# Optimization experiments

Measured on AMD Instinct MI355X. Metric: run time of the kernel, lower is better.

The kernel has to match this reference:

```python
import jax, jax.numpy as jnp
import numpy as np

N_NODES = 100000
N_EDGES = 1600000
IN_CH, HID_CH, OUT_CH = 128, 128, 64


def gcn_conv(x, edge_index, W, b, n_nodes):
    """PyG-style GCNConv: add self-loops, symmetric deg^-1/2 normalization,
    linear transform, scatter-add aggregation, bias."""
    src, dst = edge_index[0], edge_index[1]
    loop = jnp.arange(n_nodes, dtype=src.dtype)
    src = jnp.concatenate([src, loop])
    dst = jnp.concatenate([dst, loop])
    # degree computed on destination side (includes self-loops)
    deg = jax.ops.segment_sum(jnp.ones_like(dst, dtype=x.dtype), dst,
                              num_segments=n_nodes)
    dinv = jnp.where(deg > 0, jax.lax.rsqrt(deg), jnp.zeros_like(deg))
    norm = dinv[src] * dinv[dst]            # [E+N]
    h = x @ W                               # [N, out] transform before aggregate
    msg = h[src] * norm[:, None]            # [E+N, out] gathered+scaled messages
    out = jax.ops.segment_sum(msg, dst, num_segments=n_nodes)
    return out + b


def setup_inputs() -> dict:
    key = jax.random.key(0)
    ks = jax.random.split(key, 6)
    x = jax.random.normal(ks[0], (N_NODES, IN_CH), dtype=jnp.float32)
    pos_edge_index = jax.random.randint(ks[1], (2, N_EDGES), 0, N_NODES, dtype=jnp.int64)
    neg_edge_index = jax.random.randint(ks[2], (2, N_EDGES), 0, N_NODES, dtype=jnp.int64)
    # Glorot-ish init for weights
    W1 = jax.random.normal(ks[3], (IN_CH, HID_CH), dtype=jnp.float32) / np.sqrt(IN_CH)
    b1 = jnp.zeros((HID_CH,), dtype=jnp.float32)
    W2 = jax.random.normal(ks[4], (HID_CH, OUT_CH), dtype=jnp.float32) / np.sqrt(HID_CH)
    b2 = jnp.zeros((OUT_CH,), dtype=jnp.float32)
    return {"x": x, "pos_edge_index": pos_edge_index,
            "neg_edge_index": neg_edge_index,
            "W1": W1, "b1": b1, "W2": W2, "b2": b2}


def reference(x, pos_edge_index, neg_edge_index, W1, b1, W2, b2):
    n = x.shape[0]
    # encode: conv1 -> relu -> conv2 (message passing uses pos_edge_index)
    h = gcn_conv(x, pos_edge_index, W1, b1, n)
    h = jax.nn.relu(h)
    z = gcn_conv(h, pos_edge_index, W2, b2, n)
    # decode: gather node pairs, elementwise mul, sum over feature dim
    pos_pred = jnp.sum(z[pos_edge_index[0]] * z[pos_edge_index[1]], axis=1)
    neg_pred = jnp.sum(z[neg_edge_index[0]] * z[neg_edge_index[1]], axis=1)
    return (pos_pred, neg_pred)
```

## Files before the change

kernel.cpp:

```cpp
#include <hip/hip_runtime.h>


#define IC1 128
#define OC1 128
#define OC2 64

#define BSH    9
#define BNODES (1 << BSH)
#define NBMAX  512
#define CHB    4096
#define CHH    4096

typedef unsigned int u32;
typedef unsigned short u16;
typedef __attribute__((ext_vector_type(8))) short short8v;
typedef __attribute__((ext_vector_type(4))) float f32x4;

__device__ __forceinline__ u16 f2bf(float f) {
  u32 u = __float_as_uint(f);
  u32 r = (u + 0x7fffu + ((u >> 16) & 1u)) >> 16;
  return (u16)r;
}
__device__ __forceinline__ u32 pack2bf(float lo, float hi) {
  return (u32)f2bf(lo) | ((u32)f2bf(hi) << 16);
}
__device__ __forceinline__ float bflo(u32 w) { return __uint_as_float(w << 16); }
__device__ __forceinline__ float bfhi(u32 w) { return __uint_as_float(w & 0xffff0000u); }

__device__ __forceinline__ int getIdx(const void* p, long long i, int is64) {
  return is64 ? (int)((const long long*)p)[i] : ((const int*)p)[i];
}

__global__ void k_detect(const void* pei, long long E, int n_nodes, int* flagbuf,
                         int* bcnt, int* gcur0, int NB) {
  __shared__ int bad;
  if (threadIdx.x == 0) bad = 0;
  __syncthreads();
  long long cnt = E < 4096 ? E : 4096;
  const unsigned long long* p64 = (const unsigned long long*)pei;
  for (long long i = threadIdx.x; i < cnt; i += blockDim.x)
    if (p64[i] >= (unsigned long long)n_nodes) bad = 1;
  for (int i = threadIdx.x; i < NB; i += blockDim.x) { bcnt[i] = 0; gcur0[i] = 0; }
  __syncthreads();
  if (threadIdx.x == 0) flagbuf[0] = bad ? 0 : 1;
}

__global__ __launch_bounds__(256) void k_hist(const void* pei, long long E,
                                              const int* flagbuf, int* bcnt, int NB) {
  __shared__ int h[NBMAX];
  int f = flagbuf[0];
  for (int i = threadIdx.x; i < NB; i += 256) h[i] = 0;
  __syncthreads();
  long long e0 = (long long)blockIdx.x * CHH;
  long long e1 = min(E, e0 + CHH);
  for (long long e = e0 + threadIdx.x; e < e1; e += 256)
    atomicAdd(&h[getIdx(pei, E + e, f) >> BSH], 1);
  __syncthreads();
  for (int i = threadIdx.x; i < NB; i += 256)
    if (h[i]) atomicAdd(&bcnt[i], h[i]);
}

__global__ __launch_bounds__(256) void k_bin(const void* pei, long long E,
                                             const int* flagbuf, const int* bcnt,
                                             int* gcur0, u32* binned, int NB) {
  __shared__ u32 stage[CHB];
  __shared__ int h[NBMAX], lofs[NBMAX + 1], cur[NBMAX], gofs[NBMAX], gboff[NBMAX];
  __shared__ int sa[256];
  __shared__ int carryS;
  int f = flagbuf[0];
  int tid = threadIdx.x;
  for (int i = tid; i < NB; i += 256) h[i] = 0;
  if (tid == 0) carryS = 0;
  __syncthreads();
  long long e0 = (long long)blockIdx.x * CHB;
  long long e1 = min(E, e0 + CHB);
  int cc = (int)(e1 - e0);
  for (long long e = e0 + tid; e < e1; e += 256)
    atomicAdd(&h[getIdx(pei, E + e, f) >> BSH], 1);
  __syncthreads();
  for (int base = 0; base < NB; base += 256) {
    int i = base + tid;
    int v = (i < NB) ? h[i] : 0;
    sa[tid] = v;
    __syncthreads();
    for (int off = 1; off < 256; off <<= 1) {
      int t = (tid >= off) ? sa[tid - off] : 0;
      __syncthreads();
      sa[tid] += t;
      __syncthreads();
    }
    int exc = sa[tid] - v + carryS;
    if (i < NB) { lofs[i] = exc; cur[i] = exc; }
    __syncthreads();
    if (tid == 255) carryS += sa[255];
    __syncthreads();
  }
  if (tid == 0) { lofs[NB] = cc; carryS = 0; }
  __syncthreads();
  for (int base = 0; base < NB; base += 256) {
    int i = base + tid;
    int v = (i < NB) ? bcnt[i] : 0;
    sa[tid] = v;
    __syncthreads();
    for (int off = 1; off < 256; off <<= 1) {
      int t = (tid >= off) ? sa[tid - off] : 0;
      __syncthreads();
      sa[tid] += t;
      __syncthreads();
    }
    int exc = sa[tid] - v + carryS;
    if (i < NB) gboff[i] = exc;
    __syncthreads();
    if (tid == 255) carryS += sa[255];
    __syncthreads();
  }
  for (long long e = e0 + tid; e < e1; e += 256) {
    int s = getIdx(pei, e, f);
    int d = getIdx(pei, E + e, f);
    int b = d >> BSH;
    int p = atomicAdd(&cur[b], 1);
    stage[p] = (u32)s | ((u32)(d & (BNODES - 1)) << 20);
  }
  __syncthreads();
  for (int b = tid; b < NB; b += 256) {
    int cnt = cur[b] - lofs[b];
    gofs[b] = cnt ? (gboff[b] + atomicAdd(&gcur0[b], cnt) - lofs[b]) : 0;
  }
  __syncthreads();
  for (int i = tid; i < cc; i += 256) {
    int lo = 0, hi = NB;
    while (hi - lo > 1) {
      int mid = (lo + hi) >> 1;
      if (lofs[mid] <= i) lo = mid; else hi = mid;
    }
    binned[(long long)i + gofs[lo]] = stage[i];
  }
}

__global__ __launch_bounds__(512) void k_fill2(const u32* __restrict__ binned,
                                               const int* __restrict__ bcnt,
                                               float* __restrict__ dinv,
                                               int* __restrict__ rowst,
                                               u32* __restrict__ csr, int N, int NB) {
  __shared__ int cnt[BNODES], sa[BNODES], sb[BNODES], cursor[BNODES];
  __shared__ int redu[8];
  __shared__ int baseS;
  int b = blockIdx.x;
  int v0 = b << BSH;
  int nv = min(BNODES, N - v0);
  int tid = threadIdx.x;
  int part = 0;
  for (int i = tid; i < b; i += 512) part += bcnt[i];
  #pragma unroll
  for (int off = 32; off; off >>= 1) part += __shfl_down(part, off);
  if ((tid & 63) == 0) redu[tid >> 6] = part;
  for (int i = tid; i < BNODES; i += 512) cnt[i] = 0;
  __syncthreads();
  if (tid == 0) {
    int s = 0;
    #pragma unroll
    for (int w = 0; w < 8; ++w) s += redu[w];
    baseS = s;
  }
  __syncthreads();
  int base = baseS;
  int j1 = base + bcnt[b];
  for (int j = base + tid; j < j1; j += 512)
    atomicAdd(&cnt[binned[j] >> 20], 1);
  __syncthreads();
  sa[tid] = cnt[tid];
  __syncthreads();
  int* A = sa; int* B = sb;
  #pragma unroll 1
  for (int off = 1; off < BNODES; off <<= 1) {
    B[tid] = A[tid] + ((tid >= off) ? A[tid - off] : 0);
    __syncthreads();
    int* t = A; A = B; B = t;
  }
  if (tid < nv) {
    int c = cnt[tid];
    int exc = A[tid] - c;
    rowst[v0 + tid] = base + exc;
    cursor[tid] = exc;
    dinv[v0 + tid] = rsqrtf((float)(c + 1));
  }
  if (b == NB - 1 && tid == 0) rowst[N] = j1;
  __syncthreads();
  for (int j = base + tid; j < j1; j += 512) {
    u32 u = binned[j];
    int p = atomicAdd(&cursor[u >> 20], 1);
    csr[base + p] = u & 0xFFFFFu;
  }
}

__global__ void k_prepw(const float* __restrict__ W1, const float* __restrict__ W2,
                        u16* __restrict__ Wt1, u16* __restrict__ Wt2) {
  int i = blockIdx.x * blockDim.x + threadIdx.x;
  if (i < 128 * OC1) {
    int k = i / OC1, c = i % OC1;
    Wt1[c * 128 + k] = f2bf(W1[i]);
  } else {
    int j = i - 128 * OC1;
    if (j < 128 * OC2) {
      int k = j / OC2, c = j % OC2;
      Wt2[c * 128 + k] = f2bf(W2[j]);
    }
  }
}

template<int OC, bool BF16IN>
__global__ __launch_bounds__(256) void k_gemm_mfma(const void* __restrict__ xin,
                                                   const u16* __restrict__ Wt,
                                                   u16* __restrict__ t, int N) {
  constexpr int CT = OC / 16;
  constexpr int LW = 136;
  __shared__ u16 xs[128][LW];
  const int tid = threadIdx.x;
  const int lane = tid & 63, wv = tid >> 6;
  const long long rowBase = (long long)blockIdx.x * 128;

  if constexpr (BF16IN) {
    const u16* xg = (const u16*)xin;
    #pragma unroll
    for (int i = tid; i < 128 * 16; i += 256) {
      int r = i >> 4, c = i & 15;
      uint4 v = make_uint4(0u, 0u, 0u, 0u);
      if (rowBase + r < N) v = ((const uint4*)(xg + (rowBase + r) * IC1))[c];
      *(uint4*)&xs[r][c * 8] = v;
    }
  } else {
    const float* xg = (const float*)xin;
    #pragma unroll
    for (int i = tid; i < 128 * 16; i += 256) {
      int r = i >> 4, c = i & 15;
      uint4 o = make_uint4(0u, 0u, 0u, 0u);
      if (rowBase + r < N) {
        const float4* src = (const float4*)(xg + (rowBase + r) * IC1 + c * 8);
        float4 a = src[0], bq = src[1];
        o.x = pack2bf(a.x, a.y);  o.y = pack2bf(a.z, a.w);
        o.z = pack2bf(bq.x, bq.y); o.w = pack2bf(bq.z, bq.w);
      }
      *(uint4*)&xs[r][c * 8] = o;
    }
  }
  __syncthreads();

  const int frow = lane & 15, fk = (lane >> 4) * 8;
  short8v a[2][4];
  #pragma unroll
  for (int rt = 0; rt < 2; ++rt)
    #pragma unroll
    for (int kq = 0; kq < 4; ++kq)
      a[rt][kq] = *(const short8v*)&xs[wv * 32 + rt * 16 + frow][kq * 32 + fk];

  f32x4 acc[2][CT];
  #pragma unroll
  for (int ct = 0; ct < CT; ++ct) {
    acc[0][ct] = (f32x4){0.f, 0.f, 0.f, 0.f};
    acc[1][ct] = (f32x4){0.f, 0.f, 0.f, 0.f};
    #pragma unroll
    for (int kq = 0; kq < 4; ++kq) {
      short8v bfrag = *(const short8v*)(Wt + (ct * 16 + frow) * 128 + kq * 32 + fk);
      acc[0][ct] = __builtin_amdgcn_mfma_f32_16x16x32_bf16(a[0][kq], bfrag, acc[0][ct], 0, 0, 0);
      acc[1][ct] = __builtin_amdgcn_mfma_f32_16x16x32_bf16(a[1][kq], bfrag, acc[1][ct], 0, 0, 0);
    }
  }

  const int crow0 = (lane >> 4) * 4, ccol = lane & 15;
  #pragma unroll
  for (int rt = 0; rt < 2; ++rt)
    #pragma unroll
    for (int ct = 0; ct < CT; ++ct)
      #pragma unroll
      for (int r = 0; r < 4; ++r) {
        long long row = rowBase + wv * 32 + rt * 16 + crow0 + r;
        if (row < N) t[row * OC + ct * 16 + ccol] = f2bf(acc[rt][ct][r]);
      }
}

template<int CH>
__global__ __launch_bounds__(256) void k_agg(const u16* __restrict__ t,
                                             u16* __restrict__ out,
                                             const float* __restrict__ dinv,
                                             const int* __restrict__ rowst,
                                             const u32* __restrict__ csr,
                                             const float* __restrict__ bias,
                                             int N, int relu) {
  constexpr int G   = CH / 8;
  constexpr int EPI = 64 / G;
  long long wid = ((long long)blockIdx.x * blockDim.x + threadIdx.x) >> 6;
  int lane = threadIdx.x & 63;
  if (wid >= N) return;
  int v = (int)wid;
  int sub = lane / G;
  int cl  = lane % G;
  float dv = dinv[v];
  float selfw = (sub == 0) ? dv * dv : 0.f;
  float acc[8];
  {
    uint4 u = ((const uint4*)(t + (long long)v * CH))[cl];
    acc[0] = bflo(u.x) * selfw; acc[1] = bfhi(u.x) * selfw;
    acc[2] = bflo(u.y) * selfw; acc[3] = bfhi(u.y) * selfw;
    acc[4] = bflo(u.z) * selfw; acc[5] = bfhi(u.z) * selfw;
    acc[6] = bflo(u.w) * selfw; acc[7] = bfhi(u.w) * selfw;
  }
  int st = rowst[v];
  int cnt = rowst[v + 1] - st;
  for (int base = 0; base < cnt; base += 64) {
    int m = min(64, cnt - base);
    int s = 0; float w = 0.f;
    if (lane < m) { s = (int)csr[st + base + lane]; w = dinv[s] * dv; }
    int iters = (m + EPI - 1) / EPI;
    #pragma unroll 4
    for (int j = 0; j < iters; ++j) {
      int src  = __shfl(s, j * EPI + sub);
      float ww = __shfl(w, j * EPI + sub);
      uint4 u = ((const uint4*)(t + (long long)src * CH))[cl];
      acc[0] += bflo(u.x) * ww; acc[1] += bfhi(u.x) * ww;
      acc[2] += bflo(u.y) * ww; acc[3] += bfhi(u.y) * ww;
      acc[4] += bflo(u.z) * ww; acc[5] += bfhi(u.z) * ww;
      acc[6] += bflo(u.w) * ww; acc[7] += bfhi(u.w) * ww;
    }
  }
  #pragma unroll
  for (int off = G; off < 64; off <<= 1) {
    #pragma unroll
    for (int i = 0; i < 8; ++i) acc[i] += __shfl_xor(acc[i], off);
  }
  if (sub == 0) {
    float4 b0 = ((const float4*)bias)[cl * 2];
    float4 b1 = ((const float4*)bias)[cl * 2 + 1];
    float o[8] = {acc[0] + b0.x, acc[1] + b0.y, acc[2] + b0.z, acc[3] + b0.w,
                  acc[4] + b1.x, acc[5] + b1.y, acc[6] + b1.z, acc[7] + b1.w};
    if (relu) {
      #pragma unroll
      for (int i = 0; i < 8; ++i) o[i] = fmaxf(o[i], 0.f);
    }
    uint4 w4;
    w4.x = pack2bf(o[0], o[1]); w4.y = pack2bf(o[2], o[3]);
    w4.z = pack2bf(o[4], o[5]); w4.w = pack2bf(o[6], o[7]);
    ((uint4*)(out + (long long)v * CH))[cl] = w4;
  }
}

__global__ __launch_bounds__(256) void k_decode(const u16* __restrict__ z,
                                                const void* pei, const void* nei,
                                                float* __restrict__ out,
                                                long long E, const int* flagbuf) {
  int f = flagbuf[0];
  long long g = ((long long)blockIdx.x * blockDim.x + threadIdx.x) >> 3;
  int wi = threadIdx.x & 7;
  if (g >= 2 * E) return;
  const void* ei = (g < E) ? pei : nei;
  long long e = (g < E) ? g : g - E;
  int s = getIdx(ei, e, f);
  int d = getIdx(ei, E + e, f);
  uint4 a = ((const uint4*)(z + (long long)s * OC2))[wi];
  uint4 b = ((const uint4*)(z + (long long)d * OC2))[wi];
  float p = bflo(a.x) * bflo(b.x) + bfhi(a.x) * bfhi(b.x)
          + bflo(a.y) * bflo(b.y) + bfhi(a.y) * bfhi(b.y)
          + bflo(a.z) * bflo(b.z) + bfhi(a.z) * bfhi(b.z)
          + bflo(a.w) * bflo(b.w) + bfhi(a.w) * bfhi(b.w);
  p += __shfl_xor(p, 4);
  p += __shfl_xor(p, 2);
  p += __shfl_xor(p, 1);
  if (wi == 0) out[g] = p;
}

extern "C" void kernel_launch(void* const* d_in, const int* in_sizes, int n_in,
                              void* d_out, int out_size, void* d_ws, size_t ws_size,
                              hipStream_t stream) {
  const float* x  = (const float*)d_in[0];
  const void*  pei = d_in[1];
  const void*  nei = d_in[2];
  const float* W1 = (const float*)d_in[3];
  const float* b1 = (const float*)d_in[4];
  const float* W2 = (const float*)d_in[5];
  const float* b2 = (const float*)d_in[6];
  float* out = (float*)d_out;

  const int       N  = in_sizes[0] / IC1;
  const long long E  = in_sizes[1] / 2;
  const int       NB = (N + BNODES - 1) >> BSH;

  char* p = (char*)d_ws;
  auto carve = [&](size_t bytes) { char* r = p; p += ((bytes + 255) & ~(size_t)255); return r; };
  int*   flagbuf = (int*)  carve(8);
  float* dinv    = (float*)carve((size_t)N * 4);
  int*   rowst   = (int*)  carve((size_t)(N + 1) * 4);
  int*   bcnt    = (int*)  carve((size_t)NB * 4);
  int*   gcur0   = (int*)  carve((size_t)NB * 4);
  u32*   binned  = (u32*)  carve((size_t)E * 4);
  u32*   csr     = (u32*)  carve((size_t)E * 4);
  u16*   Wt1     = (u16*)  carve((size_t)128 * OC1 * 2);
  u16*   Wt2     = (u16*)  carve((size_t)128 * OC2 * 2);
  u16*   bufA    = (u16*)  carve((size_t)N * IC1 * 2);
  u16*   bufB    = (u16*)  carve((size_t)N * IC1 * 2);

  const int B = 256;

  k_detect<<<1, B, 0, stream>>>(pei, E, N, flagbuf, bcnt, gcur0, NB);
  k_hist<<<dim3((unsigned)((E + CHH - 1) / CHH)), B, 0, stream>>>(pei, E, flagbuf,
                                                                  bcnt, NB);
  k_bin<<<dim3((unsigned)((E + CHB - 1) / CHB)), B, 0, stream>>>(pei, E, flagbuf,
                                                                 bcnt, gcur0,
                                                                 binned, NB);
  k_fill2<<<dim3(NB), 512, 0, stream>>>(binned, bcnt, dinv, rowst, csr, N, NB);

  k_prepw<<<dim3((128 * (OC1 + OC2) + B - 1) / B), B, 0, stream>>>(W1, W2, Wt1, Wt2);

  k_gemm_mfma<OC1, false><<<dim3((N + 127) / 128), B, 0, stream>>>(x, Wt1, bufA, N);
  k_agg<OC1><<<dim3((N + 3) / 4), B, 0, stream>>>(bufA, bufB, dinv, rowst,
                                                  csr, b1, N, 1);

  k_gemm_mfma<OC2, true><<<dim3((N + 127) / 128), B, 0, stream>>>(bufB, Wt2, bufA, N);
  k_agg<OC2><<<dim3((N + 3) / 4), B, 0, stream>>>(bufA, bufB, dinv, rowst,
                                                  csr, b2, N, 0);

  long long groups = 2 * E;
  dim3 gD((unsigned)((groups * 8 + B - 1) / B));
  k_decode<<<gD, B, 0, stream>>>(bufB, pei, nei, out, E, flagbuf);
}
```

Measured before the change: 412.7 us.

## Scatter binned edges directly to global instead of staging through LDS

The binning kernel no longer builds a local prefix scan and LDS staging buffer. It reserves a global range per bucket up front, then scatters each edge straight to global memory using an LDS atomic offset. This removes one scan pass, the staging copy and a binary search per element, at the cost of less coalesced global writes. Counter zeroing moves from the detect kernel to hipMemsetAsync, and the detect sample shrinks to 512 entries.

```diff
diff --git a/kernel.cpp b/kernel.cpp
--- a/kernel.cpp
+++ b/kernel.cpp
@@ -31,16 +31,14 @@
   return is64 ? (int)((const long long*)p)[i] : ((const int*)p)[i];
 }
 
-__global__ void k_detect(const void* pei, long long E, int n_nodes, int* flagbuf,
-                         int* bcnt, int* gcur0, int NB) {
+__global__ void k_detect(const void* pei, long long E, int n_nodes, int* flagbuf) {
   __shared__ int bad;
   if (threadIdx.x == 0) bad = 0;
   __syncthreads();
-  long long cnt = E < 4096 ? E : 4096;
+  long long cnt = E < 512 ? E : 512;
   const unsigned long long* p64 = (const unsigned long long*)pei;
   for (long long i = threadIdx.x; i < cnt; i += blockDim.x)
     if (p64[i] >= (unsigned long long)n_nodes) bad = 1;
-  for (int i = threadIdx.x; i < NB; i += blockDim.x) { bcnt[i] = 0; gcur0[i] = 0; }
   __syncthreads();
   if (threadIdx.x == 0) flagbuf[0] = bad ? 0 : 1;
 }
@@ -63,8 +61,7 @@
 __global__ __launch_bounds__(256) void k_bin(const void* pei, long long E,
                                              const int* flagbuf, const int* bcnt,
                                              int* gcur0, u32* binned, int NB) {
-  __shared__ u32 stage[CHB];
-  __shared__ int h[NBMAX], lofs[NBMAX + 1], cur[NBMAX], gofs[NBMAX], gboff[NBMAX];
+  __shared__ int h[NBMAX], gstart[NBMAX], gboff[NBMAX];
   __shared__ int sa[256];
   __shared__ int carryS;
   int f = flagbuf[0];
@@ -74,28 +71,8 @@
   __syncthreads();
   long long e0 = (long long)blockIdx.x * CHB;
   long long e1 = min(E, e0 + CHB);
-  int cc = (int)(e1 - e0);
   for (long long e = e0 + tid; e < e1; e += 256)
     atomicAdd(&h[getIdx(pei, E + e, f) >> BSH], 1);
-  __syncthreads();
-  for (int base = 0; base < NB; base += 256) {
-    int i = base + tid;
-    int v = (i < NB) ? h[i] : 0;
-    sa[tid] = v;
-    __syncthreads();
-    for (int off = 1; off < 256; off <<= 1) {
-      int t = (tid >= off) ? sa[tid - off] : 0;
-      __syncthreads();
-      sa[tid] += t;
-      __syncthreads();
-    }
-    int exc = sa[tid] - v + carryS;
-    if (i < NB) { lofs[i] = exc; cur[i] = exc; }
-    __syncthreads();
-    if (tid == 255) carryS += sa[255];
-    __syncthreads();
-  }
-  if (tid == 0) { lofs[NB] = cc; carryS = 0; }
   __syncthreads();
   for (int base = 0; base < NB; base += 256) {
     int i = base + tid;
@@ -114,26 +91,18 @@
     if (tid == 255) carryS += sa[255];
     __syncthreads();
   }
+  for (int b = tid; b < NB; b += 256) {
+    int c = h[b];
+    gstart[b] = c ? (gboff[b] + atomicAdd(&gcur0[b], c)) : 0;
+    h[b] = 0;
+  }
+  __syncthreads();
   for (long long e = e0 + tid; e < e1; e += 256) {
     int s = getIdx(pei, e, f);
     int d = getIdx(pei, E + e, f);
     int b = d >> BSH;
-    int p = atomicAdd(&cur[b], 1);
-    stage[p] = (u32)s | ((u32)(d & (BNODES - 1)) << 20);
-  }
-  __syncthreads();
-  for (int b = tid; b < NB; b += 256) {
-    int cnt = cur[b] - lofs[b];
-    gofs[b] = cnt ? (gboff[b] + atomicAdd(&gcur0[b], cnt) - lofs[b]) : 0;
-  }
-  __syncthreads();
-  for (int i = tid; i < cc; i += 256) {
-    int lo = 0, hi = NB;
-    while (hi - lo > 1) {
-      int mid = (lo + hi) >> 1;
-      if (lofs[mid] <= i) lo = mid; else hi = mid;
-    }
-    binned[(long long)i + gofs[lo]] = stage[i];
+    int ofs = atomicAdd(&h[b], 1);
+    binned[(long long)gstart[b] + ofs] = (u32)s | ((u32)(d & (BNODES - 1)) << 20);
   }
 }
 
@@ -399,7 +368,9 @@
 
   const int B = 256;
 
-  k_detect<<<1, B, 0, stream>>>(pei, E, N, flagbuf, bcnt, gcur0, NB);
+  hipMemsetAsync(bcnt, 0, (size_t)NB * 4, stream);
+  hipMemsetAsync(gcur0, 0, (size_t)NB * 4, stream);
+  k_detect<<<1, B, 0, stream>>>(pei, E, N, flagbuf);
   k_hist<<<dim3((unsigned)((E + CHH - 1) / CHH)), B, 0, stream>>>(pei, E, flagbuf,
                                                                   bcnt, NB);
   k_bin<<<dim3((unsigned)((E + CHB - 1) / CHB)), B, 0, stream>>>(pei, E, flagbuf,
```

After: 413.2 us. About the same (+0.1%).
